# Kernel optimization log

Hardware: AMD Instinct MI355X
Metric: run time of the kernel (lower is better)

The kernel has to match this reference:

```python
import jax, jax.numpy as jnp
import numpy as np

RNN = 400
K_WIN = 10      # num_window_mixtures
N_MIX = 20      # num_mixtures
ALPHA = 80      # alphabet_size
IN2 = RNN + ALPHA + 3  # lstm2/lstm3 input size = 483
MDN_OUT = 1 + 6 * N_MIX  # 121


def setup_inputs() -> dict:
    key = jax.random.key(0)
    ks = jax.random.split(key, 20)
    std = 0.075
    B, T, U = 256, 800, 100
    inp = {
        "trajectory": jax.random.normal(ks[0], (B, T, 3), jnp.float32),
        "char_sequence": jax.random.uniform(ks[1], (B, U, ALPHA), jnp.float32),
        # LSTM1 (input 3)
        "w_ih1": jax.random.normal(ks[2], (4 * RNN, 3), jnp.float32) * std,
        "w_hh1": jax.random.normal(ks[3], (4 * RNN, RNN), jnp.float32) * std,
        "b1": jax.random.normal(ks[4], (4 * RNN,), jnp.float32) * std,
        # LSTM2 (input 483)
        "w_ih2": jax.random.normal(ks[5], (4 * RNN, IN2), jnp.float32) * std,
        "w_hh2": jax.random.normal(ks[6], (4 * RNN, RNN), jnp.float32) * std,
        "b2": jax.random.normal(ks[7], (4 * RNN,), jnp.float32) * std,
        # LSTM3 (input 483)
        "w_ih3": jax.random.normal(ks[8], (4 * RNN, IN2), jnp.float32) * std,
        "w_hh3": jax.random.normal(ks[9], (4 * RNN, RNN), jnp.float32) * std,
        "b3": jax.random.normal(ks[10], (4 * RNN,), jnp.float32) * std,
        # window linear (Graves attention), bias init mean -3.0 std 0.25
        "w_win": jax.random.normal(ks[11], (3 * K_WIN, RNN), jnp.float32) * std,
        "b_win": jax.random.normal(ks[12], (3 * K_WIN,), jnp.float32) * 0.25 - 3.0,
        # MDN head
        "w_mdn": jax.random.normal(ks[13], (MDN_OUT, RNN), jnp.float32) * std,
        "b_mdn": jax.random.normal(ks[14], (MDN_OUT,), jnp.float32) * std,
    }
    return inp


def _lstm_cell(x, h, c, w_ih, w_hh, b):
    # torch.nn.LSTMCell gate order: i, f, g, o
    gates = x @ w_ih.T + h @ w_hh.T + b
    i, f, g, o = jnp.split(gates, 4, axis=-1)
    c_new = jax.nn.sigmoid(f) * c + jax.nn.sigmoid(i) * jnp.tanh(g)
    h_new = jax.nn.sigmoid(o) * jnp.tanh(c_new)
    return h_new, c_new


def reference(trajectory, char_sequence,
              w_ih1, w_hh1, b1, w_ih2, w_hh2, b2, w_ih3, w_hh3, b3,
              w_win, b_win, w_mdn, b_mdn):
    B, T, _ = trajectory.shape
    U = char_sequence.shape[1]
    u = jnp.arange(U, dtype=trajectory.dtype)  # [U]

    def step(carry, x_t):
        h1, c1, h2, c2, h3, c3, kappa = carry
        h1, c1 = _lstm_cell(x_t, h1, c1, w_ih1, w_hh1, b1)
        # Gaussian-window attention
        wp = jnp.exp(h1 @ w_win.T + b_win).reshape(B, 3, K_WIN)
        alpha, beta, dkappa = wp[:, 0], wp[:, 1], wp[:, 2]
        kappa = kappa + dkappa
        # phi: [B, U] = sum_k alpha_k * exp(-beta_k * (kappa_k - u)^2)
        diff = kappa[:, :, None] - u[None, None, :]          # [B, K, U]
        phi = jnp.sum(alpha[:, :, None] * jnp.exp(-beta[:, :, None] * diff * diff), axis=1)
        window = jnp.einsum('bu,bua->ba', phi, char_sequence)  # [B, ALPHA]
        x2 = jnp.concatenate([h1, window, x_t], axis=1)
        h2, c2 = _lstm_cell(x2, h2, c2, w_ih2, w_hh2, b2)
        x3 = jnp.concatenate([h2, window, x_t], axis=1)
        h3, c3 = _lstm_cell(x3, h3, c3, w_ih3, w_hh3, b3)
        out = h3 @ w_mdn.T + b_mdn  # [B, 121]
        return (h1, c1, h2, c2, h3, c3, kappa), out

    z = jnp.zeros((B, RNN), trajectory.dtype)
    kappa0 = jnp.zeros((B, K_WIN), trajectory.dtype)
    carry0 = (z, z, z, z, z, z, kappa0)
    _, outs = jax.lax.scan(step, carry0, jnp.swapaxes(trajectory, 0, 1))  # [T, B, 121]
    return jnp.swapaxes(outs, 0, 1)  # [B, T, 121]
```

## Files before the change

kernel.cpp:

```cpp
#include <hip/hip_runtime.h>
#include <hip/hip_bf16.h>

#define RNNU 400
#define NBATCH 256
#define TT 800
#define UU 100
#define ALW 80
#define KW 10
#define K1 416
#define K2 896
#define NBLK 256
#define NTHR 256

typedef unsigned short u16;
typedef unsigned int u32;
typedef unsigned long long u64;
typedef __attribute__((ext_vector_type(8))) short bfrag;
typedef __attribute__((ext_vector_type(4))) float f4;

constexpr long P1 = (long)NBATCH * K1;
constexpr long P2 = (long)NBATCH * K2;
constexpr long WP1 = 1600L * K1;
constexpr long WP2 = 1600L * K2;
constexpr long WPM = 128L * K1;
constexpr long WPW = 32L * K1;
constexpr long NCB = (long)NBATCH * UU * ALW;

constexpr size_t OFF_FLAGS = 0;
constexpr size_t OFF_U1 = 16384;
constexpr size_t OFF_U2 = OFF_U1 + (size_t)4 * P1 * 2;
constexpr size_t OFF_U3 = OFF_U2 + (size_t)4 * P2 * 2;
constexpr size_t OFF_W1 = OFF_U3 + (size_t)4 * P2 * 2;
constexpr size_t OFF_W2 = OFF_W1 + (size_t)2 * WP1 * 2;
constexpr size_t OFF_W3 = OFF_W2 + (size_t)2 * WP2 * 2;
constexpr size_t OFF_WM = OFF_W3 + (size_t)2 * WP2 * 2;
constexpr size_t OFF_WW = OFF_WM + (size_t)2 * WPM * 2;
constexpr size_t OFF_PB1 = OFF_WW + (size_t)2 * WPW * 2;
constexpr size_t OFF_PB2 = OFF_PB1 + 6400;
constexpr size_t OFF_PB3 = OFF_PB2 + 6400;
constexpr size_t OFF_C1 = OFF_PB3 + 6400;
constexpr size_t OFF_C2 = OFF_C1 + 409600;
constexpr size_t OFF_C3 = OFF_C2 + 409600;
constexpr size_t OFF_KP = OFF_C3 + 409600;
constexpr size_t OFF_CB = OFF_KP + 16384;

__device__ __forceinline__ u16 f2b(float x) {
  union { float f; u32 u; } v; v.f = x;
  u32 r = (v.u + 0x7FFFu + ((v.u >> 16) & 1u)) >> 16;
  return (u16)r;
}
__device__ __forceinline__ float b2f(u16 h) {
  union { u32 u; float f; } q; q.u = ((u32)h) << 16; return q.f;
}
__device__ __forceinline__ void wsp2(u16* base, long plane, long idx, float v) {
  u16 hi = f2b(v);
  base[idx] = hi;
  base[plane + idx] = f2b(v - b2f(hi));
}
__device__ __forceinline__ void wsp2c(u16* base, long plane, long idx, float v) {
  u16 hi = f2b(v);
  __hip_atomic_store(base + idx, hi, __ATOMIC_RELAXED, __HIP_MEMORY_SCOPE_AGENT);
  __hip_atomic_store(base + plane + idx, f2b(v - b2f(hi)), __ATOMIC_RELAXED, __HIP_MEMORY_SCOPE_AGENT);
}
__device__ __forceinline__ void st_coh16(u16* p, u16 v) {
  __hip_atomic_store(p, v, __ATOMIC_RELAXED, __HIP_MEMORY_SCOPE_AGENT);
}
__device__ __forceinline__ bfrag ld_frag_coh(const u16* p) {
  u64 lo = __hip_atomic_load((const u64*)p, __ATOMIC_RELAXED, __HIP_MEMORY_SCOPE_AGENT);
  u64 hi = __hip_atomic_load((const u64*)(p + 4), __ATOMIC_RELAXED, __HIP_MEMORY_SCOPE_AGENT);
  union { u64 q[2]; bfrag f; } u; u.q[0] = lo; u.q[1] = hi; return u.f;
}
__device__ __forceinline__ float sigf(float x) { return 1.f / (1.f + __expf(-x)); }
__device__ __forceinline__ float tanhf_(float x) {
  float e = __expf(-2.f * x); return (1.f - e) / (1.f + e);
}

__global__ void prep_kernel(
    const float* __restrict__ w_ih1, const float* __restrict__ w_hh1, const float* __restrict__ b1,
    const float* __restrict__ w_ih2, const float* __restrict__ w_hh2, const float* __restrict__ b2,
    const float* __restrict__ w_ih3, const float* __restrict__ w_hh3, const float* __restrict__ b3,
    const float* __restrict__ w_win, const float* __restrict__ w_mdn,
    const float* __restrict__ traj, const float* __restrict__ chars, char* __restrict__ ws)
{
  u16* W1 = (u16*)(ws + OFF_W1);
  u16* W2 = (u16*)(ws + OFF_W2);
  u16* W3 = (u16*)(ws + OFF_W3);
  u16* WM = (u16*)(ws + OFF_WM);
  u16* WW = (u16*)(ws + OFF_WW);
  u16* CB = (u16*)(ws + OFF_CB);

  const long N1 = WP1, N2 = WP2, N3 = WP2;
  const long N4 = WPM, N5 = WPW, N6 = 4800, N7 = 307200, N8 = 2560, N9 = 4096;
  const long N10 = P1, N11 = (long)NBATCH * RNNU, N12 = (long)NBATCH * RNNU, N13 = NCB;
  const long total = N1 + N2 + N3 + N4 + N5 + N6 + N7 + N8 + N9 + N10 + N11 + N12 + N13;

  for (long i = (long)blockIdx.x * blockDim.x + threadIdx.x; i < total;
       i += (long)gridDim.x * blockDim.x) {
    long j = i;
    if (j < N1) { int n = (int)(j / K1), k = (int)(j % K1);
      int s = (n & 3) * 400 + (n >> 2);
      float v = (k < 3) ? w_ih1[s * 3 + k] : ((k >= 16) ? w_hh1[(long)s * 400 + (k - 16)] : 0.f);
      wsp2(W1, WP1, j, v); continue; } j -= N1;
    if (j < N2) { int n = (int)(j / K2), k = (int)(j % K2);
      int s = (n & 3) * 400 + (n >> 2);
      float v = (k < 483) ? w_ih2[(long)s * 483 + k] : ((k >= 496) ? w_hh2[(long)s * 400 + (k - 496)] : 0.f);
      wsp2(W2, WP2, j, v); continue; } j -= N2;
    if (j < N3) { int n = (int)(j / K2), k = (int)(j % K2);
      int s = (n & 3) * 400 + (n >> 2);
      float v = (k < 483) ? w_ih3[(long)s * 483 + k] : ((k >= 496) ? w_hh3[(long)s * 400 + (k - 496)] : 0.f);
      wsp2(W3, WP2, j, v); continue; } j -= N3;
    if (j < N4) { int n = (int)(j / K1), k = (int)(j % K1);
      float v = (n < 121 && k >= 16) ? w_mdn[(long)n * 400 + (k - 16)] : 0.f;
      wsp2(WM, WPM, j, v); continue; } j -= N4;
    if (j < N5) { int n = (int)(j / K1), k = (int)(j % K1);
      float v = (n < 30 && k < 400) ? w_win[(long)n * 400 + k] : 0.f;
      wsp2(WW, WPW, j, v); continue; } j -= N5;
    if (j < N6) { int w = (int)(j / 1600), n = (int)(j % 1600);
      int s = (n & 3) * 400 + (n >> 2);
      float* pb = (float*)(ws + (w == 0 ? OFF_PB1 : (w == 1 ? OFF_PB2 : OFF_PB3)));
      const float* bb = (w == 0 ? b1 : (w == 1 ? b2 : b3));
      pb[n] = bb[s]; continue; } j -= N6;
    if (j < N7) { ((float*)(ws + OFF_C1))[j] = 0.f; continue; } j -= N7;
    if (j < N8) { ((float*)(ws + OFF_KP))[j] = 0.f; continue; } j -= N8;
    if (j < N9) { ((u32*)(ws + OFF_FLAGS))[j] = 0u; continue; } j -= N9;
    if (j < N10) { int r = (int)(j / K1), k = (int)(j % K1);
      u16* U1 = (u16*)(ws + OFF_U1);
      float v = (k < 3) ? traj[(long)r * 2400 + k] : 0.f;
      wsp2(U1, P1, j, v); continue; } j -= N10;
    if (j < N11) { int r = (int)(j / 400), k = (int)(j % 400);
      u16* U2 = (u16*)(ws + OFF_U2);
      long idx = (long)r * K2 + 496 + k;
      U2[idx] = 0; U2[P2 + idx] = 0; continue; } j -= N11;
    if (j < N12) { int r = (int)(j / 400), k = (int)(j % 400);
      u16* U3 = (u16*)(ws + OFF_U3);
      long idx = (long)r * K2 + 496 + k;
      U3[idx] = 0; U3[P2 + idx] = 0; continue; } j -= N12;
    CB[j] = f2b(chars[j]);
  }
}

__device__ __forceinline__ void gridbar(u32* flags, u32 e, int bid, int tid) {
  asm volatile("s_waitcnt vmcnt(0)" ::: "memory");
  __syncthreads();
  if (tid == 0)
    __hip_atomic_store(&flags[bid * 16], e, __ATOMIC_RELAXED, __HIP_MEMORY_SCOPE_AGENT);
  u32* f = &flags[tid * 16];
  while (__hip_atomic_load(f, __ATOMIC_RELAXED, __HIP_MEMORY_SCOPE_AGENT) < e)
    __builtin_amdgcn_s_sleep(2);
  __syncthreads();
}

template<int NK, int KPAD>
__device__ __forceinline__ void gemm_gate_tile(
    int rt, int ct, const u16* __restrict__ Abase, long APS,
    const u16* __restrict__ Wbase, long WPS,
    const float* __restrict__ pbias, float* __restrict__ cst,
    u16* __restrict__ hd0, int st0, long ps0,
    u16* __restrict__ hd1, int st1, long ps1,
    float* __restrict__ ldsb, int lane)
{
  const int r0 = rt * 32, c0 = ct * 80;
  f4 acc[2][5];
#pragma unroll
  for (int a = 0; a < 2; a++)
#pragma unroll
    for (int b = 0; b < 5; b++) acc[a][b] = (f4)(0.f);

  const long aoff = (long)(r0 + (lane & 15)) * KPAD + ((lane >> 4) * 8);
  const long woff = (long)(c0 + (lane & 15)) * KPAD + ((lane >> 4) * 8);
  const u16* Ah0 = Abase + aoff;
  const u16* Ah1 = Ah0 + 16 * KPAD;
  const u16* Al0 = Abase + APS + aoff;
  const u16* Al1 = Al0 + 16 * KPAD;
  const u16* Wh = Wbase + woff;
  const u16* Wl = Wbase + WPS + woff;

#pragma unroll
  for (int kb = 0; kb < NK; ++kb) {
    bfrag a0 = ld_frag_coh(Ah0 + kb * 32);
    bfrag a1 = ld_frag_coh(Ah1 + kb * 32);
#pragma unroll
    for (int cf = 0; cf < 5; ++cf) {
      bfrag wh = *(const bfrag*)(Wh + (long)cf * 16 * KPAD + kb * 32);
      bfrag wl = *(const bfrag*)(Wl + (long)cf * 16 * KPAD + kb * 32);
      acc[0][cf] = __builtin_amdgcn_mfma_f32_16x16x32_bf16(a0, wh, acc[0][cf], 0, 0, 0);
      acc[1][cf] = __builtin_amdgcn_mfma_f32_16x16x32_bf16(a1, wh, acc[1][cf], 0, 0, 0);
      acc[0][cf] = __builtin_amdgcn_mfma_f32_16x16x32_bf16(a0, wl, acc[0][cf], 0, 0, 0);
      acc[1][cf] = __builtin_amdgcn_mfma_f32_16x16x32_bf16(a1, wl, acc[1][cf], 0, 0, 0);
    }
  }
#pragma unroll
  for (int kb = 0; kb < NK; ++kb) {
    bfrag a0 = ld_frag_coh(Al0 + kb * 32);
    bfrag a1 = ld_frag_coh(Al1 + kb * 32);
#pragma unroll
    for (int cf = 0; cf < 5; ++cf) {
      bfrag wh = *(const bfrag*)(Wh + (long)cf * 16 * KPAD + kb * 32);
      acc[0][cf] = __builtin_amdgcn_mfma_f32_16x16x32_bf16(a0, wh, acc[0][cf], 0, 0, 0);
      acc[1][cf] = __builtin_amdgcn_mfma_f32_16x16x32_bf16(a1, wh, acc[1][cf], 0, 0, 0);
    }
  }
  const int cl = lane & 15, rq = lane >> 4;
#pragma unroll
  for (int rf = 0; rf < 2; ++rf)
#pragma unroll
    for (int cf = 0; cf < 5; ++cf) {
      float bias = pbias[c0 + cf * 16 + cl];
#pragma unroll
      for (int r = 0; r < 4; ++r)
        ldsb[(rf * 16 + rq * 4 + r) * 80 + cf * 16 + cl] = acc[rf][cf][r] + bias;
    }
  asm volatile("s_waitcnt lgkmcnt(0)" ::: "memory");
#pragma unroll
  for (int q = 0; q < 10; ++q) {
    int idx = q * 64 + lane;
    int rl = idx / 20, ul = idx % 20;
    float gi = ldsb[rl * 80 + 4 * ul + 0];
    float gf = ldsb[rl * 80 + 4 * ul + 1];
    float gg = ldsb[rl * 80 + 4 * ul + 2];
    float go = ldsb[rl * 80 + 4 * ul + 3];
    long row = r0 + rl; int unit = ct * 20 + ul;
    long ci = row * 400 + unit;
    float cn = sigf(gf) * cst[ci] + sigf(gi) * tanhf_(gg);
    cst[ci] = cn;
    float hv = sigf(go) * tanhf_(cn);
    u16 hh = f2b(hv);
    u16 hl = f2b(hv - b2f(hh));
    long i0 = row * st0 + unit;
    st_coh16(hd0 + i0, hh); st_coh16(hd0 + ps0 + i0, hl);
    if (hd1) { long i1 = row * st1 + unit; st_coh16(hd1 + i1, hh); st_coh16(hd1 + ps1 + i1, hl); }
  }
}

__device__ __forceinline__ void mdn_tile(
    int mt, const u16* __restrict__ Abase, long APS,
    const u16* __restrict__ Wm, long WPS,
    const float* __restrict__ b_mdn, float* __restrict__ out, int tcol, int lane)
{
  const int r0 = mt * 16;
  f4 acc[8];
#pragma unroll
  for (int c = 0; c < 8; c++) acc[c] = (f4)(0.f);
  const long aoff = (long)(r0 + (lane & 15)) * K2 + ((lane >> 4) * 8);
  const long woff = (long)(lane & 15) * K1 + ((lane >> 4) * 8);
  const u16* Ah = Abase + aoff;
  const u16* Al = Abase + APS + aoff;
  const u16* Wh = Wm + woff;
  const u16* Wl = Wm + WPS + woff;
#pragma unroll
  for (int kb = 0; kb < 13; ++kb) {
    bfrag a = ld_frag_coh(Ah + kb * 32);
#pragma unroll
    for (int cf = 0; cf < 8; ++cf) {
      bfrag wh = *(const bfrag*)(Wh + (long)cf * 16 * K1 + kb * 32);
      bfrag wl = *(const bfrag*)(Wl + (long)cf * 16 * K1 + kb * 32);
      acc[cf] = __builtin_amdgcn_mfma_f32_16x16x32_bf16(a, wh, acc[cf], 0, 0, 0);
      acc[cf] = __builtin_amdgcn_mfma_f32_16x16x32_bf16(a, wl, acc[cf], 0, 0, 0);
    }
  }
#pragma unroll
  for (int kb = 0; kb < 13; ++kb) {
    bfrag a = ld_frag_coh(Al + kb * 32);
#pragma unroll
    for (int cf = 0; cf < 8; ++cf) {
      bfrag wh = *(const bfrag*)(Wh + (long)cf * 16 * K1 + kb * 32);
      acc[cf] = __builtin_amdgcn_mfma_f32_16x16x32_bf16(a, wh, acc[cf], 0, 0, 0);
    }
  }
  const int cl = lane & 15, rq = lane >> 4;
#pragma unroll
  for (int cf = 0; cf < 8; ++cf) {
    int col = cf * 16 + cl;
    if (col < 121) {
      float bias = b_mdn[col];
#pragma unroll
      for (int r = 0; r < 4; ++r) {
        long row = r0 + rq * 4 + r;
        out[(row * TT + tcol) * 121 + col] = acc[cf][r] + bias;
      }
    }
  }
}

__global__ void __launch_bounds__(NTHR) handw_kernel(
    const float* __restrict__ traj, const float* __restrict__ chars,
    const float* __restrict__ b_win, const float* __restrict__ b_mdn,
    float* __restrict__ out, char* __restrict__ ws)
{
  u32* flags = (u32*)(ws + OFF_FLAGS);
  u16* U1b = (u16*)(ws + OFF_U1);
  u16* U2b = (u16*)(ws + OFF_U2);
  u16* U3b = (u16*)(ws + OFF_U3);
  const u16* W1 = (const u16*)(ws + OFF_W1);
  const u16* W2 = (const u16*)(ws + OFF_W2);
  const u16* W3 = (const u16*)(ws + OFF_W3);
  const u16* WM = (const u16*)(ws + OFF_WM);
  const u16* WW = (const u16*)(ws + OFF_WW);
  const u16* CB = (const u16*)(ws + OFF_CB);
  const float* PB1 = (const float*)(ws + OFF_PB1);
  const float* PB2 = (const float*)(ws + OFF_PB2);
  const float* PB3 = (const float*)(ws + OFF_PB3);
  float* C1 = (float*)(ws + OFF_C1);
  float* C2 = (float*)(ws + OFF_C2);
  float* C3 = (float*)(ws + OFF_C3);
  float* KP = (float*)(ws + OFF_KP);

  __shared__ float ldseb[2][32 * 80];
  __shared__ float ldswp[16 * 32];
  __shared__ float ldsal[16 * KW];
  __shared__ float ldsbe[16 * KW];
  __shared__ float ldskp[16 * KW];
  __shared__ float ldsphi[16 * UU];

  const int bid = blockIdx.x, tid = threadIdx.x;
  const int wid = tid >> 6, lane = tid & 63;
  u32 epoch = 0;
  const int gtile = (wid < 2 && bid < 80) ? (wid * 80 + bid) : -1;
  const int rt = (gtile >= 0) ? gtile / 20 : 0;
  const int ct = (gtile >= 0) ? gtile % 20 : 0;

  for (int t = 0; t < TT; ++t) {
    const int p = t & 1;
    u16* U1p = U1b + (size_t)p * 2 * P1;
    u16* U1n = U1b + (size_t)(p ^ 1) * 2 * P1;
    u16* U2p = U2b + (size_t)p * 2 * P2;
    u16* U2n = U2b + (size_t)(p ^ 1) * 2 * P2;
    u16* U3p = U3b + (size_t)p * 2 * P2;
    u16* U3n = U3b + (size_t)(p ^ 1) * 2 * P2;

    if (gtile >= 0)
      gemm_gate_tile<13, K1>(rt, ct, U1p, P1, W1, WP1, PB1, C1,
                             U1n + 16, K1, P1, U2p, K2, P2, ldseb[wid], lane);
    if (t > 0 && wid == 0 && bid >= 80 && bid < 96)
      mdn_tile(bid - 80, U3p + 480, P2, WM, WPM, b_mdn, out, t - 1, lane);
    gridbar(flags, ++epoch, bid, tid);

    if (bid < 16) {
      const int r0 = bid * 16;
      if (wid == 0) {
        f4 wacc[2]; wacc[0] = (f4)(0.f); wacc[1] = (f4)(0.f);
        const long aoff = (long)(r0 + (lane & 15)) * K2 + ((lane >> 4) * 8);
        const long woff = (long)(lane & 15) * K1 + ((lane >> 4) * 8);
        const u16* Ah = U2p + aoff;
        const u16* Al = U2p + P2 + aoff;
        const u16* Wh = WW + woff;
        const u16* Wl = WW + WPW + woff;
#pragma unroll
        for (int kb = 0; kb < 13; ++kb) {
          bfrag a = ld_frag_coh(Ah + kb * 32);
          bfrag b0h = *(const bfrag*)(Wh + kb * 32);
          bfrag b0l = *(const bfrag*)(Wl + kb * 32);
          bfrag b1h = *(const bfrag*)(Wh + 16 * K1 + kb * 32);
          bfrag b1l = *(const bfrag*)(Wl + 16 * K1 + kb * 32);
          wacc[0] = __builtin_amdgcn_mfma_f32_16x16x32_bf16(a, b0h, wacc[0], 0, 0, 0);
          wacc[0] = __builtin_amdgcn_mfma_f32_16x16x32_bf16(a, b0l, wacc[0], 0, 0, 0);
          wacc[1] = __builtin_amdgcn_mfma_f32_16x16x32_bf16(a, b1h, wacc[1], 0, 0, 0);
          wacc[1] = __builtin_amdgcn_mfma_f32_16x16x32_bf16(a, b1l, wacc[1], 0, 0, 0);
        }
#pragma unroll
        for (int kb = 0; kb < 13; ++kb) {
          bfrag a = ld_frag_coh(Al + kb * 32);
          bfrag b0h = *(const bfrag*)(Wh + kb * 32);
          bfrag b1h = *(const bfrag*)(Wh + 16 * K1 + kb * 32);
          wacc[0] = __builtin_amdgcn_mfma_f32_16x16x32_bf16(a, b0h, wacc[0], 0, 0, 0);
          wacc[1] = __builtin_amdgcn_mfma_f32_16x16x32_bf16(a, b1h, wacc[1], 0, 0, 0);
        }
        const int cl = lane & 15, rq = lane >> 4;
#pragma unroll
        for (int cf = 0; cf < 2; ++cf) {
          int col = cf * 16 + cl;
          float bias = (col < 30) ? b_win[col] : 0.f;
#pragma unroll
          for (int r = 0; r < 4; ++r)
            ldswp[(rq * 4 + r) * 32 + col] = wacc[cf][r] + bias;
        }
      }
      __syncthreads();
      if (tid < 160) {
        int r = tid / 10, k = tid % 10; int row = r0 + r;
        float kap = KP[row * 10 + k] + __expf(ldswp[r * 32 + 20 + k]);
        KP[row * 10 + k] = kap;
        ldskp[r * 10 + k] = kap;
        ldsal[r * 10 + k] = __expf(ldswp[r * 32 + k]);
        ldsbe[r * 10 + k] = __expf(ldswp[r * 32 + 10 + k]);
      } else if (tid < 208) {
        int q = tid - 160; int r = q / 3, c = q % 3; int row = r0 + r;
        float xv = traj[((long)row * TT + t) * 3 + c];
        wsp2c(U2p, P2, (long)row * K2 + 480 + c, xv);
        wsp2c(U3p, P2, (long)row * K2 + 480 + c, xv);
        if (t + 1 < TT)
          wsp2c(U1n, P1, (long)row * K1 + c, traj[((long)row * TT + t + 1) * 3 + c]);
      }
      __syncthreads();
      {
        int r = tid & 15, uq = tid >> 4;
        for (int u = uq; u < UU; u += 16) {
          float s = 0.f;
#pragma unroll
          for (int k = 0; k < KW; ++k) {
            float d = ldskp[r * 10 + k] - (float)u;
            s += ldsal[r * 10 + k] * __expf(-ldsbe[r * 10 + k] * d * d);
          }
          ldsphi[r * UU + u] = s;
        }
      }
      __syncthreads();
      {
        int r = tid >> 4, d0 = tid & 15; int row = r0 + r;
        float w[5] = {0.f, 0.f, 0.f, 0.f, 0.f};
        const u16* cb = CB + (long)row * UU * ALW;
#pragma unroll 4
        for (int u = 0; u < UU; ++u) {
          float ph = ldsphi[r * UU + u];
#pragma unroll
          for (int jj = 0; jj < 5; ++jj) w[jj] += ph * b2f(cb[u * ALW + d0 + 16 * jj]);
        }
#pragma unroll
        for (int jj = 0; jj < 5; ++jj) {
          int d = d0 + 16 * jj;
          wsp2c(U2p, P2, (long)row * K2 + 400 + d, w[jj]);
          wsp2c(U3p, P2, (long)row * K2 + 400 + d, w[jj]);
        }
      }
    }
    gridbar(flags, ++epoch, bid, tid);

    if (gtile >= 0)
      gemm_gate_tile<28, K2>(rt, ct, U2p, P2, W2, WP2, PB2, C2,
                             U3p, K2, P2, U2n + 496, K2, P2, ldseb[wid], lane);
    gridbar(flags, ++epoch, bid, tid);

    if (gtile >= 0)
      gemm_gate_tile<28, K2>(rt, ct, U3p, P2, W3, WP2, PB3, C3,
                             U3n + 496, K2, P2, (u16*)nullptr, 0, 0, ldseb[wid], lane);
    gridbar(flags, ++epoch, bid, tid);
  }
  if (wid == 0 && bid >= 80 && bid < 96)
    mdn_tile(bid - 80, U3b + 480, P2, WM, WPM, b_mdn, out, TT - 1, lane);
}

extern "C" void kernel_launch(void* const* d_in, const int* in_sizes, int n_in,
                              void* d_out, int out_size, void* d_ws, size_t ws_size,
                              hipStream_t stream) {
  const float* traj   = (const float*)d_in[0];
  const float* chars  = (const float*)d_in[1];
  const float* w_ih1  = (const float*)d_in[2];
  const float* w_hh1  = (const float*)d_in[3];
  const float* b1     = (const float*)d_in[4];
  const float* w_ih2  = (const float*)d_in[5];
  const float* w_hh2  = (const float*)d_in[6];
  const float* b2     = (const float*)d_in[7];
  const float* w_ih3  = (const float*)d_in[8];
  const float* w_hh3  = (const float*)d_in[9];
  const float* b3     = (const float*)d_in[10];
  const float* w_win  = (const float*)d_in[11];
  const float* b_win  = (const float*)d_in[12];
  const float* w_mdn  = (const float*)d_in[13];
  const float* b_mdn  = (const float*)d_in[14];
  float* outp = (float*)d_out;
  char* wsp = (char*)d_ws;

  prep_kernel<<<dim3(8192), dim3(256), 0, stream>>>(
      w_ih1, w_hh1, b1, w_ih2, w_hh2, b2, w_ih3, w_hh3, b3, w_win, w_mdn, traj, chars, wsp);

  void* kargs[] = { (void*)&traj, (void*)&chars, (void*)&b_win, (void*)&b_mdn,
                    (void*)&outp, (void*)&wsp };
  hipError_t err = hipLaunchCooperativeKernel((void*)handw_kernel, dim3(NBLK), dim3(NTHR),
                                              kargs, 0, stream);
  if (err != hipSuccess) {
    handw_kernel<<<dim3(NBLK), dim3(NTHR), 0, stream>>>(traj, chars, b_win, b_mdn, outp, wsp);
  }
}
```

Measured before the change: 321.6 ms.

## Shrink persistent grid to 96 blocks, use counter barrier, read chars directly

Cuts the cooperative persistent grid from 256 to 96 blocks. The per-block flag-array barrier becomes a single atomic-counter barrier with a release word. Removes the bf16 copy of char_sequence so the window sum reads fp32 chars directly. The goal is lower per-timestep barrier cost across 800 steps with fewer participants. The risk is that gate GEMM tiles indexed by gtile may rely on there being more blocks, which would change work coverage.

```diff
diff --git a/kernel.cpp b/kernel.cpp
--- a/kernel.cpp
+++ b/kernel.cpp
@@ -9,7 +9,7 @@
 #define KW 10
 #define K1 416
 #define K2 896
-#define NBLK 256
+#define NBLK 96
 #define NTHR 256
 
 typedef unsigned short u16;
@@ -24,7 +24,6 @@
 constexpr long WP2 = 1600L * K2;
 constexpr long WPM = 128L * K1;
 constexpr long WPW = 32L * K1;
-constexpr long NCB = (long)NBATCH * UU * ALW;
 
 constexpr size_t OFF_FLAGS = 0;
 constexpr size_t OFF_U1 = 16384;
@@ -42,7 +41,6 @@
 constexpr size_t OFF_C2 = OFF_C1 + 409600;
 constexpr size_t OFF_C3 = OFF_C2 + 409600;
 constexpr size_t OFF_KP = OFF_C3 + 409600;
-constexpr size_t OFF_CB = OFF_KP + 16384;
 
 __device__ __forceinline__ u16 f2b(float x) {
   union { float f; u32 u; } v; v.f = x;
@@ -80,19 +78,18 @@
     const float* __restrict__ w_ih2, const float* __restrict__ w_hh2, const float* __restrict__ b2,
     const float* __restrict__ w_ih3, const float* __restrict__ w_hh3, const float* __restrict__ b3,
     const float* __restrict__ w_win, const float* __restrict__ w_mdn,
-    const float* __restrict__ traj, const float* __restrict__ chars, char* __restrict__ ws)
+    const float* __restrict__ traj, char* __restrict__ ws)
 {
   u16* W1 = (u16*)(ws + OFF_W1);
   u16* W2 = (u16*)(ws + OFF_W2);
   u16* W3 = (u16*)(ws + OFF_W3);
   u16* WM = (u16*)(ws + OFF_WM);
   u16* WW = (u16*)(ws + OFF_WW);
-  u16* CB = (u16*)(ws + OFF_CB);
 
   const long N1 = WP1, N2 = WP2, N3 = WP2;
   const long N4 = WPM, N5 = WPW, N6 = 4800, N7 = 307200, N8 = 2560, N9 = 4096;
-  const long N10 = P1, N11 = (long)NBATCH * RNNU, N12 = (long)NBATCH * RNNU, N13 = NCB;
-  const long total = N1 + N2 + N3 + N4 + N5 + N6 + N7 + N8 + N9 + N10 + N11 + N12 + N13;
+  const long N10 = P1, N11 = (long)NBATCH * RNNU, N12 = (long)NBATCH * RNNU;
+  const long total = N1 + N2 + N3 + N4 + N5 + N6 + N7 + N8 + N9 + N10 + N11 + N12;
 
   for (long i = (long)blockIdx.x * blockDim.x + threadIdx.x; i < total;
        i += (long)gridDim.x * blockDim.x) {
@@ -131,22 +128,25 @@
       u16* U2 = (u16*)(ws + OFF_U2);
       long idx = (long)r * K2 + 496 + k;
       U2[idx] = 0; U2[P2 + idx] = 0; continue; } j -= N11;
-    if (j < N12) { int r = (int)(j / 400), k = (int)(j % 400);
+    { int r = (int)(j / 400), k = (int)(j % 400);
       u16* U3 = (u16*)(ws + OFF_U3);
       long idx = (long)r * K2 + 496 + k;
-      U3[idx] = 0; U3[P2 + idx] = 0; continue; } j -= N12;
-    CB[j] = f2b(chars[j]);
-  }
-}
-
-__device__ __forceinline__ void gridbar(u32* flags, u32 e, int bid, int tid) {
+      U3[idx] = 0; U3[P2 + idx] = 0; }
+  }
+}
+
+__device__ __forceinline__ void gridbar(u32* bar, u32 target, int tid) {
   asm volatile("s_waitcnt vmcnt(0)" ::: "memory");
   __syncthreads();
-  if (tid == 0)
-    __hip_atomic_store(&flags[bid * 16], e, __ATOMIC_RELAXED, __HIP_MEMORY_SCOPE_AGENT);
-  u32* f = &flags[tid * 16];
-  while (__hip_atomic_load(f, __ATOMIC_RELAXED, __HIP_MEMORY_SCOPE_AGENT) < e)
-    __builtin_amdgcn_s_sleep(2);
+  if (tid == 0) {
+    u32 old = __hip_atomic_fetch_add(&bar[0], 1u, __ATOMIC_RELAXED, __HIP_MEMORY_SCOPE_AGENT);
+    if (old == target * NBLK - 1u) {
+      __hip_atomic_store(&bar[16], target, __ATOMIC_RELAXED, __HIP_MEMORY_SCOPE_AGENT);
+    } else {
+      while (__hip_atomic_load(&bar[16], __ATOMIC_RELAXED, __HIP_MEMORY_SCOPE_AGENT) < target)
+        __builtin_amdgcn_s_sleep(2);
+    }
+  }
   __syncthreads();
 }
 
@@ -287,7 +287,7 @@
     const float* __restrict__ b_win, const float* __restrict__ b_mdn,
     float* __restrict__ out, char* __restrict__ ws)
 {
-  u32* flags = (u32*)(ws + OFF_FLAGS);
+  u32* bar = (u32*)(ws + OFF_FLAGS);
   u16* U1b = (u16*)(ws + OFF_U1);
   u16* U2b = (u16*)(ws + OFF_U2);
   u16* U3b = (u16*)(ws + OFF_U3);
@@ -296,7 +296,6 @@
   const u16* W3 = (const u16*)(ws + OFF_W3);
   const u16* WM = (const u16*)(ws + OFF_WM);
   const u16* WW = (const u16*)(ws + OFF_WW);
-  const u16* CB = (const u16*)(ws + OFF_CB);
   const float* PB1 = (const float*)(ws + OFF_PB1);
   const float* PB2 = (const float*)(ws + OFF_PB2);
   const float* PB3 = (const float*)(ws + OFF_PB3);
@@ -333,7 +332,7 @@
                              U1n + 16, K1, P1, U2p, K2, P2, ldseb[wid], lane);
     if (t > 0 && wid == 0 && bid >= 80 && bid < 96)
       mdn_tile(bid - 80, U3p + 480, P2, WM, WPM, b_mdn, out, t - 1, lane);
-    gridbar(flags, ++epoch, bid, tid);
+    gridbar(bar, ++epoch, tid);
 
     if (bid < 16) {
       const int r0 = bid * 16;
@@ -408,12 +407,12 @@
       {
         int r = tid >> 4, d0 = tid & 15; int row = r0 + r;
         float w[5] = {0.f, 0.f, 0.f, 0.f, 0.f};
-        const u16* cb = CB + (long)row * UU * ALW;
+        const float* cb = chars + (long)row * UU * ALW;
 #pragma unroll 4
         for (int u = 0; u < UU; ++u) {
           float ph = ldsphi[r * UU + u];
 #pragma unroll
-          for (int jj = 0; jj < 5; ++jj) w[jj] += ph * b2f(cb[u * ALW + d0 + 16 * jj]);
+          for (int jj = 0; jj < 5; ++jj) w[jj] += ph * cb[u * ALW + d0 + 16 * jj];
         }
 #pragma unroll
         for (int jj = 0; jj < 5; ++jj) {
@@ -423,17 +422,17 @@
         }
       }
     }
-    gridbar(flags, ++epoch, bid, tid);
+    gridbar(bar, ++epoch, tid);
 
     if (gtile >= 0)
       gemm_gate_tile<28, K2>(rt, ct, U2p, P2, W2, WP2, PB2, C2,
                              U3p, K2, P2, U2n + 496, K2, P2, ldseb[wid], lane);
-    gridbar(flags, ++epoch, bid, tid);
+    gridbar(bar, ++epoch, tid);
 
     if (gtile >= 0)
       gemm_gate_tile<28, K2>(rt, ct, U3p, P2, W3, WP2, PB3, C3,
                              U3n + 496, K2, P2, (u16*)nullptr, 0, 0, ldseb[wid], lane);
-    gridbar(flags, ++epoch, bid, tid);
+    gridbar(bar, ++epoch, tid);
   }
   if (wid == 0 && bid >= 80 && bid < 96)
     mdn_tile(bid - 80, U3b + 480, P2, WM, WPM, b_mdn, out, TT - 1, lane);
@@ -461,7 +460,7 @@
   char* wsp = (char*)d_ws;
 
   prep_kernel<<<dim3(8192), dim3(256), 0, stream>>>(
-      w_ih1, w_hh1, b1, w_ih2, w_hh2, b2, w_ih3, w_hh3, b3, w_win, w_mdn, traj, chars, wsp);
+      w_ih1, w_hh1, b1, w_ih2, w_hh2, b2, w_ih3, w_hh3, b3, w_win, w_mdn, traj, wsp);
 
   void* kargs[] = { (void*)&traj, (void*)&chars, (void*)&b_win, (void*)&b_mdn,
                     (void*)&outp, (void*)&wsp };
```

After: 340.4 ms. +5.8%, slower.
